# Kernel optimization log

Measured on AMD Instinct MI355X. Metric: run time of the kernel, lower is better.

## Reference

```python
import jax, jax.numpy as jnp
import numpy as np

B, T, D, H = 32, 1024, 512, 512


def setup_inputs() -> dict:
    key = jax.random.key(0)
    ks = jax.random.split(key, 9)
    K = 1.0 / np.sqrt(H)
    u = lambda k, s: jax.random.uniform(k, s, jnp.float32, -K, K)
    return {
        "x": jax.random.normal(ks[0], (B, T, D), jnp.float32),
        "w_ih_fw": u(ks[1], (3 * H, D)),
        "w_hh_fw": u(ks[2], (3 * H, H)),
        "b_ih_fw": u(ks[3], (3 * H,)),
        "b_hh_fw": u(ks[4], (3 * H,)),
        "w_ih_bw": u(ks[5], (3 * H, D)),
        "w_hh_bw": u(ks[6], (3 * H, H)),
        "b_ih_bw": u(ks[7], (3 * H,)),
        "b_hh_bw": u(ks[8], (3 * H,)),
    }


def _gru_scan(x, w_ih, w_hh, b_ih, b_hh, reverse):
    # x: (B, T, D) -> precompute input projections for all steps: (T, B, 3H)
    b, t, d = x.shape
    h_dim = w_hh.shape[1]
    ih = jnp.einsum("btd,gd->tbg", x, w_ih) + b_ih

    def step(h, ih_t):
        hh = h @ w_hh.T + b_hh  # (B, 3H)
        r = jax.nn.sigmoid(ih_t[:, :h_dim] + hh[:, :h_dim])
        z = jax.nn.sigmoid(ih_t[:, h_dim:2 * h_dim] + hh[:, h_dim:2 * h_dim])
        n = jnp.tanh(ih_t[:, 2 * h_dim:] + r * hh[:, 2 * h_dim:])
        h_new = (1.0 - z) * n + z * h
        return h_new, h_new

    h0 = jnp.zeros((b, h_dim), x.dtype)
    h_last, ys = jax.lax.scan(step, h0, ih, reverse=reverse)
    # ys: (T, B, H), aligned to original time indices even when reverse=True
    return jnp.transpose(ys, (1, 0, 2)), h_last


def reference(x, w_ih_fw, w_hh_fw, b_ih_fw, b_hh_fw, w_ih_bw, w_hh_bw, b_ih_bw, b_hh_bw):
    out_fw, h_fw = _gru_scan(x, w_ih_fw, w_hh_fw, b_ih_fw, b_hh_fw, reverse=False)
    out_bw, h_bw = _gru_scan(x, w_ih_bw, w_hh_bw, b_ih_bw, b_hh_bw, reverse=True)
    outputs = jnp.concatenate([out_fw, out_bw], axis=-1)  # (B, T, 2H)
    return outputs, h_fw, h_bw
```

## Files before the change

### kernel.cpp

```cpp
#include <hip/hip_runtime.h>


#define T_LEN 1024
#define B_SZ  32
#define D_SZ  512
#define H_SZ  512
#define NWG_DIR 32
#define JW 16
#define NTHR 512

typedef __attribute__((ext_vector_type(8))) _Float16 half8;
typedef __attribute__((ext_vector_type(4))) float f32x4;
typedef __attribute__((ext_vector_type(4))) int int4v;

__device__ __forceinline__ _Float16 f2h(float f) { return (_Float16)f; }
__device__ __forceinline__ float sigm_f(float v) {
  return __builtin_amdgcn_rcpf(1.f + __expf(-v));
}
__device__ __forceinline__ float tanh_f(float v) {
  return 1.f - 2.f * __builtin_amdgcn_rcpf(1.f + __expf(2.f * v));
}
__device__ __forceinline__ void bar_lgkm() {
  asm volatile("s_waitcnt lgkmcnt(0)\ns_barrier" ::: "memory");
}

__global__ __launch_bounds__(NTHR, 2)
void gru2_persistent(const float* __restrict__ x,
                     const float* __restrict__ wih_fw, const float* __restrict__ whh_fw,
                     const float* __restrict__ bih_fw, const float* __restrict__ bhh_fw,
                     const float* __restrict__ wih_bw, const float* __restrict__ whh_bw,
                     const float* __restrict__ bih_bw, const float* __restrict__ bhh_bw,
                     float* __restrict__ out,
                     unsigned long long* __restrict__ hex64,
                     unsigned* __restrict__ flags)
{
  __shared__ float Cp[24 * 272];
  __shared__ float biasLds[96];
  __shared__ unsigned long long hLds64[B_SZ * 4];
  unsigned* hLds = (unsigned*)hLds64;

  const int bid  = blockIdx.x;
  const int dir  = bid >> 5;
  const int g    = bid & 31;
  const int tid  = threadIdx.x;
  const int wave = tid >> 6;
  const int lane = tid & 63;

  const float* wih = dir ? wih_bw : wih_fw;
  const float* whh = dir ? whh_bw : whh_fw;
  const float* bih = dir ? bih_bw : bih_fw;
  const float* bhh = dir ? bhh_bw : bhh_fw;

  if (tid < 48) {
    int grow = (tid >> 4) * H_SZ + g * JW + (tid & 15);
    biasLds[tid]      = bih[grow];
    biasLds[48 + tid] = bhh[grow];
  }

  const bool isHh = (wave >= 4);
  const int  wv   = wave & 3;
  const int  wm   = wv & 1;
  const int  kh   = wv >> 1;

  half8 Bf[3][8];
  {
    const float* W = isHh ? whh : wih;
    #pragma unroll
    for (int gam = 0; gam < 3; ++gam) {
      const int row = gam * H_SZ + g * JW + (lane & 15);
      #pragma unroll
      for (int i = 0; i < 8; ++i) {
        const float* src = W + (size_t)row * D_SZ + (kh * 8 + i) * 32 + ((lane >> 4) << 3);
        float4 v0 = *(const float4*)(src);
        float4 v1 = *(const float4*)(src + 4);
        half8 b;
        b[0]=f2h(v0.x); b[1]=f2h(v0.y); b[2]=f2h(v0.z); b[3]=f2h(v0.w);
        b[4]=f2h(v1.x); b[5]=f2h(v1.y); b[6]=f2h(v1.z); b[7]=f2h(v1.w);
        Bf[gam][i] = b;
      }
    }
  }

  const int arow = wm * 16 + (lane & 15);
  const int koff = (lane >> 4) << 3;

  float4 xn[16];
  if (!isHh) {
    const int t0 = dir ? (T_LEN - 1) : 0;
    const float* base = x + ((size_t)arow * T_LEN + t0) * D_SZ + kh * 256 + koff;
    #pragma unroll
    for (int i = 0; i < 8; ++i) {
      xn[2*i]   = *(const float4*)(base + i * 32);
      xn[2*i+1] = *(const float4*)(base + i * 32 + 4);
    }
  }
  __syncthreads();

  float hreg = 0.f;
  const int gb = tid >> 4;
  const int gj = tid & 15;
  float* hlast = out + (size_t)B_SZ * T_LEN * (2 * H_SZ) + (size_t)dir * B_SZ * H_SZ;
  const unsigned* flbase = flags + (size_t)dir * NWG_DIR;

  for (int s = 0; s < T_LEN; ++s) {
    const int t = dir ? (T_LEN - 1 - s) : s;
    const bool hasNext = (s + 1 < T_LEN);

    f32x4 acc[3] = {{0.f,0.f,0.f,0.f},{0.f,0.f,0.f,0.f},{0.f,0.f,0.f,0.f}};

    if (!isHh) {
      half8 a[8];
      #pragma unroll
      for (int i = 0; i < 8; ++i) {
        float4 u = xn[2*i], w = xn[2*i+1];
        half8 h;
        h[0]=f2h(u.x); h[1]=f2h(u.y); h[2]=f2h(u.z); h[3]=f2h(u.w);
        h[4]=f2h(w.x); h[5]=f2h(w.y); h[6]=f2h(w.z); h[7]=f2h(w.w);
        a[i] = h;
      }
      if (hasNext) {
        const int tn = dir ? (T_LEN - 2 - s) : (s + 1);
        const float* base = x + ((size_t)arow * T_LEN + tn) * D_SZ + kh * 256 + koff;
        #pragma unroll
        for (int i = 0; i < 8; ++i) {
          xn[2*i]   = *(const float4*)(base + i * 32);
          xn[2*i+1] = *(const float4*)(base + i * 32 + 4);
        }
      }
      #pragma unroll
      for (int i = 0; i < 8; ++i)
        #pragma unroll
        for (int gam = 0; gam < 3; ++gam)
          acc[gam] = __builtin_amdgcn_mfma_f32_16x16x32_f16(a[i], Bf[gam][i], acc[gam], 0, 0, 0);
    } else if (s > 0) {
      for (;;) {
        unsigned v = (lane < NWG_DIR)
            ? __hip_atomic_load(&flbase[lane], __ATOMIC_RELAXED,
                                __HIP_MEMORY_SCOPE_AGENT)
            : 0xFFFFFFFFu;
        if (__all(v >= (unsigned)s)) break;
      }
      const char* p0 = (const char*)hex64
          + (((size_t)dir * 2 + ((s - 1) & 1)) * (B_SZ * 128)) * 8
          + (size_t)arow * 1024 + (size_t)kh * 512 + (size_t)koff * 2;
      int4v hv[8];
      asm volatile(
        "global_load_dwordx4 %0, %8, off sc0 sc1\n\t"
        "global_load_dwordx4 %1, %8, off offset:64 sc0 sc1\n\t"
        "global_load_dwordx4 %2, %8, off offset:128 sc0 sc1\n\t"
        "global_load_dwordx4 %3, %8, off offset:192 sc0 sc1\n\t"
        "global_load_dwordx4 %4, %8, off offset:256 sc0 sc1\n\t"
        "global_load_dwordx4 %5, %8, off offset:320 sc0 sc1\n\t"
        "global_load_dwordx4 %6, %8, off offset:384 sc0 sc1\n\t"
        "global_load_dwordx4 %7, %8, off offset:448 sc0 sc1\n\t"
        "s_waitcnt vmcnt(0)"
        : "=&v"(hv[0]), "=&v"(hv[1]), "=&v"(hv[2]), "=&v"(hv[3]),
          "=&v"(hv[4]), "=&v"(hv[5]), "=&v"(hv[6]), "=&v"(hv[7])
        : "v"(p0) : "memory");
      __builtin_amdgcn_sched_barrier(0);
      #pragma unroll
      for (int i = 0; i < 8; ++i) {
        half8 a = __builtin_bit_cast(half8, hv[i]);
        #pragma unroll
        for (int gam = 0; gam < 3; ++gam)
          acc[gam] = __builtin_amdgcn_mfma_f32_16x16x32_f16(a, Bf[gam][i], acc[gam], 0, 0, 0);
      }
    }

    {
      const int src = isHh ? 1 : 0;
      #pragma unroll
      for (int gam = 0; gam < 3; ++gam) {
        float* cp = Cp + (size_t)(((src*2 + kh)*3 + gam)*2 + wm) * 272
                       + ((lane >> 4) << 2) * 17 + (lane & 15);
        #pragma unroll
        for (int vv2 = 0; vv2 < 4; ++vv2) cp[vv2 * 17] = acc[gam][vv2];
      }
    }
    bar_lgkm();

    float hnS;
    {
      const int mb = gb >> 4, rb = gb & 15;
      float sih[3], shh[3];
      #pragma unroll
      for (int gam = 0; gam < 3; ++gam) {
        float aih = 0.f, ahh = 0.f;
        #pragma unroll
        for (int q = 0; q < 2; ++q) {
          aih += Cp[(size_t)(((0*2+q)*3+gam)*2 + mb) * 272 + rb * 17 + gj];
          ahh += Cp[(size_t)(((1*2+q)*3+gam)*2 + mb) * 272 + rb * 17 + gj];
        }
        sih[gam] = aih + biasLds[gam * 16 + gj];
        shh[gam] = ahh + biasLds[48 + gam * 16 + gj];
      }
      const float r = sigm_f(sih[0] + shh[0]);
      const float z = sigm_f(sih[1] + shh[1]);
      const float n = tanh_f(sih[2] + r * shh[2]);
      const float hn = (1.f - z) * n + z * hreg;
      hreg = hn;
      hnS = hn;

      const float hother = __shfl_xor(hn, 1);
      if ((gj & 1) == 0) {
        union { unsigned u; _Float16 h[2]; } pr;
        pr.h[0] = f2h(hn); pr.h[1] = f2h(hother);
        hLds[gb * 8 + (gj >> 1)] = pr.u;
      }
      if (!isHh) {
        out[((size_t)gb * T_LEN + t) * (2 * H_SZ) + dir * H_SZ + g * JW + gj] = hn;
        if (s == T_LEN - 1) hlast[gb * H_SZ + g * JW + gj] = hn;
      }
    }
    bar_lgkm();

    if (wave == 4) {
      const size_t pb = ((size_t)dir * 2 + (s & 1)) * (B_SZ * 128);
      #pragma unroll
      for (int i = 0; i < 2; ++i) {
        const int id2 = i * 64 + lane;
        const int gbp = id2 >> 2, jp = id2 & 3;
        __hip_atomic_store(&hex64[pb + (size_t)gbp * 128 + g * 4 + jp],
                           hLds64[gbp * 4 + jp],
                           __ATOMIC_RELAXED, __HIP_MEMORY_SCOPE_AGENT);
      }
      asm volatile("s_waitcnt vmcnt(0)" ::: "memory");
      if (lane == 0)
        __hip_atomic_store((unsigned*)&flags[(size_t)dir * NWG_DIR + g],
                           (unsigned)(s + 1),
                           __ATOMIC_RELAXED, __HIP_MEMORY_SCOPE_AGENT);
    }
    if (isHh) {
      out[((size_t)gb * T_LEN + t) * (2 * H_SZ) + dir * H_SZ + g * JW + gj] = hnS;
      if (s == T_LEN - 1) hlast[gb * H_SZ + g * JW + gj] = hnS;
    }
  }
}

extern "C" void kernel_launch(void* const* d_in, const int* in_sizes, int n_in,
                              void* d_out, int out_size, void* d_ws, size_t ws_size,
                              hipStream_t stream) {
  const float* x      = (const float*)d_in[0];
  const float* wih_fw = (const float*)d_in[1];
  const float* whh_fw = (const float*)d_in[2];
  const float* bih_fw = (const float*)d_in[3];
  const float* bhh_fw = (const float*)d_in[4];
  const float* wih_bw = (const float*)d_in[5];
  const float* whh_bw = (const float*)d_in[6];
  const float* bih_bw = (const float*)d_in[7];
  const float* bhh_bw = (const float*)d_in[8];
  float* out = (float*)d_out;

  const size_t FLAGS_BYTES = 256;
  const size_t HEX_BYTES   = (size_t)2 * 2 * B_SZ * 128 * sizeof(unsigned long long);
  if (ws_size < FLAGS_BYTES + HEX_BYTES) return;

  unsigned* flags = (unsigned*)d_ws;
  unsigned long long* hex64 = (unsigned long long*)((char*)d_ws + FLAGS_BYTES);

  hipMemsetAsync(flags, 0, FLAGS_BYTES, stream);
  gru2_persistent<<<dim3(64), dim3(NTHR), 0, stream>>>(
      x, wih_fw, whh_fw, bih_fw, bhh_fw, wih_bw, whh_bw, bih_bw, bhh_bw,
      out, hex64, flags);
}
```

Baseline: 4.861 ms.

## Publish hidden state directly from registers and poll flags with one wave

Each step's fp16 hidden-state chunk is now packed with lane shuffles and written straight to global memory as 16-byte stores in a new fragment-friendly layout. This removes the LDS staging buffer and the single-wave copy-out stage. Only wave 4 polls the cross-workgroup flags, with a short sleep between polls, and it releases the other hh waves through a shared-memory token, so fewer waves hit the flag cache lines. The flag store is moved after a combined vmcnt/lgkmcnt barrier. This trades a lighter handoff for an extra intra-block spin and a vmcnt wait before every barrier.

```diff
diff --git a/kernel.cpp b/kernel.cpp
--- a/kernel.cpp
+++ b/kernel.cpp
@@ -31,13 +31,12 @@
                      const float* __restrict__ wih_bw, const float* __restrict__ whh_bw,
                      const float* __restrict__ bih_bw, const float* __restrict__ bhh_bw,
                      float* __restrict__ out,
-                     unsigned long long* __restrict__ hex64,
+                     char* __restrict__ hexF,
                      unsigned* __restrict__ flags)
 {
   __shared__ float Cp[24 * 272];
   __shared__ float biasLds[96];
-  __shared__ unsigned long long hLds64[B_SZ * 4];
-  unsigned* hLds = (unsigned*)hLds64;
+  __shared__ int tok;
 
   const int bid  = blockIdx.x;
   const int dir  = bid >> 5;
@@ -51,6 +50,7 @@
   const float* bih = dir ? bih_bw : bih_fw;
   const float* bhh = dir ? bhh_bw : bhh_fw;
 
+  if (tid == 0) tok = 0;
   if (tid < 48) {
     int grow = (tid >> 4) * H_SZ + g * JW + (tid & 15);
     biasLds[tid]      = bih[grow];
@@ -101,6 +101,7 @@
   const int gj = tid & 15;
   float* hlast = out + (size_t)B_SZ * T_LEN * (2 * H_SZ) + (size_t)dir * B_SZ * H_SZ;
   const unsigned* flbase = flags + (size_t)dir * NWG_DIR;
+  char* const exbase = hexF + (size_t)dir * 2 * 32768;
 
   for (int s = 0; s < T_LEN; ++s) {
     const int t = dir ? (T_LEN - 1 - s) : s;
@@ -133,30 +134,27 @@
         for (int gam = 0; gam < 3; ++gam)
           acc[gam] = __builtin_amdgcn_mfma_f32_16x16x32_f16(a[i], Bf[gam][i], acc[gam], 0, 0, 0);
     } else if (s > 0) {
-      for (;;) {
-        unsigned v = (lane < NWG_DIR)
-            ? __hip_atomic_load(&flbase[lane], __ATOMIC_RELAXED,
-                                __HIP_MEMORY_SCOPE_AGENT)
-            : 0xFFFFFFFFu;
-        if (__all(v >= (unsigned)s)) break;
-      }
-      const char* p0 = (const char*)hex64
-          + (((size_t)dir * 2 + ((s - 1) & 1)) * (B_SZ * 128)) * 8
-          + (size_t)arow * 1024 + (size_t)kh * 512 + (size_t)koff * 2;
+      if (wave == 4) {
+        for (;;) {
+          unsigned v = (lane < NWG_DIR)
+              ? __hip_atomic_load(&flbase[lane], __ATOMIC_RELAXED,
+                                  __HIP_MEMORY_SCOPE_AGENT)
+              : 0xFFFFFFFFu;
+          if (__all(v >= (unsigned)s)) break;
+          __builtin_amdgcn_s_sleep(1);
+        }
+        if (lane == 0) *((volatile int*)&tok) = s;
+      } else {
+        while (*((volatile int*)&tok) < s) __builtin_amdgcn_s_sleep(1);
+      }
+      const char* pb = exbase + (size_t)((s - 1) & 1) * 32768;
+      const char* a0 = pb + ((size_t)(kh * 32 + (lane >> 4)) * 512) + (size_t)arow * 16;
       int4v hv[8];
-      asm volatile(
-        "global_load_dwordx4 %0, %8, off sc0 sc1\n\t"
-        "global_load_dwordx4 %1, %8, off offset:64 sc0 sc1\n\t"
-        "global_load_dwordx4 %2, %8, off offset:128 sc0 sc1\n\t"
-        "global_load_dwordx4 %3, %8, off offset:192 sc0 sc1\n\t"
-        "global_load_dwordx4 %4, %8, off offset:256 sc0 sc1\n\t"
-        "global_load_dwordx4 %5, %8, off offset:320 sc0 sc1\n\t"
-        "global_load_dwordx4 %6, %8, off offset:384 sc0 sc1\n\t"
-        "global_load_dwordx4 %7, %8, off offset:448 sc0 sc1\n\t"
-        "s_waitcnt vmcnt(0)"
-        : "=&v"(hv[0]), "=&v"(hv[1]), "=&v"(hv[2]), "=&v"(hv[3]),
-          "=&v"(hv[4]), "=&v"(hv[5]), "=&v"(hv[6]), "=&v"(hv[7])
-        : "v"(p0) : "memory");
+      #pragma unroll
+      for (int i = 0; i < 8; ++i)
+        asm volatile("global_load_dwordx4 %0, %1, off sc0 sc1"
+                     : "=&v"(hv[i]) : "v"(a0 + (size_t)i * 2048));
+      asm volatile("s_waitcnt vmcnt(0)" ::: "memory");
       __builtin_amdgcn_sched_barrier(0);
       #pragma unroll
       for (int i = 0; i < 8; ++i) {
@@ -201,39 +199,27 @@
       hreg = hn;
       hnS = hn;
 
-      const float hother = __shfl_xor(hn, 1);
-      if ((gj & 1) == 0) {
-        union { unsigned u; _Float16 h[2]; } pr;
-        pr.h[0] = f2h(hn); pr.h[1] = f2h(hother);
-        hLds[gb * 8 + (gj >> 1)] = pr.u;
-      }
-      if (!isHh) {
-        out[((size_t)gb * T_LEN + t) * (2 * H_SZ) + dir * H_SZ + g * JW + gj] = hn;
-        if (s == T_LEN - 1) hlast[gb * H_SZ + g * JW + gj] = hn;
-      }
-    }
-    bar_lgkm();
-
-    if (wave == 4) {
-      const size_t pb = ((size_t)dir * 2 + (s & 1)) * (B_SZ * 128);
-      #pragma unroll
-      for (int i = 0; i < 2; ++i) {
-        const int id2 = i * 64 + lane;
-        const int gbp = id2 >> 2, jp = id2 & 3;
-        __hip_atomic_store(&hex64[pb + (size_t)gbp * 128 + g * 4 + jp],
-                           hLds64[gbp * 4 + jp],
-                           __ATOMIC_RELAXED, __HIP_MEMORY_SCOPE_AGENT);
-      }
-      asm volatile("s_waitcnt vmcnt(0)" ::: "memory");
-      if (lane == 0)
-        __hip_atomic_store((unsigned*)&flags[(size_t)dir * NWG_DIR + g],
-                           (unsigned)(s + 1),
-                           __ATOMIC_RELAXED, __HIP_MEMORY_SCOPE_AGENT);
-    }
-    if (isHh) {
-      out[((size_t)gb * T_LEN + t) * (2 * H_SZ) + dir * H_SZ + g * JW + gj] = hnS;
-      if (s == T_LEN - 1) hlast[gb * H_SZ + g * JW + gj] = hnS;
-    }
+      const unsigned hu = (unsigned)__builtin_bit_cast(unsigned short, f2h(hn));
+      unsigned v0 = hu | ((unsigned)__shfl_xor((int)hu, 1) << 16);
+      unsigned v1 = (unsigned)__shfl_xor((int)v0, 2);
+      unsigned v2 = (unsigned)__shfl_xor((int)v0, 4);
+      unsigned v3 = (unsigned)__shfl_xor((int)v1, 4);
+      if ((lane & 7) == 0) {
+        int4v pk; pk[0] = (int)v0; pk[1] = (int)v1; pk[2] = (int)v2; pk[3] = (int)v3;
+        char* dst = exbase + (size_t)(s & 1) * 32768
+                  + (size_t)(2 * g + ((lane >> 3) & 1)) * 512
+                  + (size_t)gb * 16;
+        asm volatile("global_store_dwordx4 %0, %1, off sc0 sc1"
+                     :: "v"(dst), "v"(pk) : "memory");
+      }
+    }
+    asm volatile("s_waitcnt vmcnt(0) lgkmcnt(0)\ns_barrier" ::: "memory");
+    if (tid == 0)
+      __hip_atomic_store((unsigned*)&flags[(size_t)dir * NWG_DIR + g],
+                         (unsigned)(s + 1),
+                         __ATOMIC_RELAXED, __HIP_MEMORY_SCOPE_AGENT);
+    out[((size_t)gb * T_LEN + t) * (2 * H_SZ) + dir * H_SZ + g * JW + gj] = hnS;
+    if (s == T_LEN - 1) hlast[gb * H_SZ + g * JW + gj] = hnS;
   }
 }
 
@@ -252,14 +238,14 @@
   float* out = (float*)d_out;
 
   const size_t FLAGS_BYTES = 256;
-  const size_t HEX_BYTES   = (size_t)2 * 2 * B_SZ * 128 * sizeof(unsigned long long);
+  const size_t HEX_BYTES   = (size_t)2 * 2 * 64 * 32 * 16;
   if (ws_size < FLAGS_BYTES + HEX_BYTES) return;
 
   unsigned* flags = (unsigned*)d_ws;
-  unsigned long long* hex64 = (unsigned long long*)((char*)d_ws + FLAGS_BYTES);
+  char* hexF = (char*)d_ws + FLAGS_BYTES;
 
   hipMemsetAsync(flags, 0, FLAGS_BYTES, stream);
   gru2_persistent<<<dim3(64), dim3(NTHR), 0, stream>>>(
       x, wih_fw, whh_fw, bih_fw, bhh_fw, wih_bw, whh_bw, bih_bw, bhh_bw,
-      out, hex64, flags);
-}
+      out, hexF, flags);
+}
```

Measured after the change: 4.778 ms. About the same (-1.7%).

## Publish hidden state directly from gate threads and defer x prefetch past flag

Applied to the files above, without the earlier changes.

Gate-computing threads now write their packed fp16 hidden-state pairs straight to the global exchange buffer with atomic stores. This removes the LDS staging and the single-wave copy-out before the step flag is raised. All threads wait on their own stores, then one thread publishes the flag after the barrier. The output writes and the next-step x prefetch move after the flag publication, shortening the critical path between steps. The cost is more scattered small global stores, and a per-thread vmcnt wait that also stalls on earlier output stores.

```diff
diff --git a/kernel.cpp b/kernel.cpp
--- a/kernel.cpp
+++ b/kernel.cpp
@@ -31,13 +31,11 @@
                      const float* __restrict__ wih_bw, const float* __restrict__ whh_bw,
                      const float* __restrict__ bih_bw, const float* __restrict__ bhh_bw,
                      float* __restrict__ out,
-                     unsigned long long* __restrict__ hex64,
+                     unsigned* __restrict__ hexu,
                      unsigned* __restrict__ flags)
 {
   __shared__ float Cp[24 * 272];
   __shared__ float biasLds[96];
-  __shared__ unsigned long long hLds64[B_SZ * 4];
-  unsigned* hLds = (unsigned*)hLds64;
 
   const int bid  = blockIdx.x;
   const int dir  = bid >> 5;
@@ -83,11 +81,12 @@
 
   const int arow = wm * 16 + (lane & 15);
   const int koff = (lane >> 4) << 3;
+  const float* const xwavebase = x + (size_t)arow * T_LEN * D_SZ + kh * 256 + koff;
 
   float4 xn[16];
   if (!isHh) {
     const int t0 = dir ? (T_LEN - 1) : 0;
-    const float* base = x + ((size_t)arow * T_LEN + t0) * D_SZ + kh * 256 + koff;
+    const float* base = xwavebase + (size_t)t0 * D_SZ;
     #pragma unroll
     for (int i = 0; i < 8; ++i) {
       xn[2*i]   = *(const float4*)(base + i * 32);
@@ -117,15 +116,6 @@
         h[0]=f2h(u.x); h[1]=f2h(u.y); h[2]=f2h(u.z); h[3]=f2h(u.w);
         h[4]=f2h(w.x); h[5]=f2h(w.y); h[6]=f2h(w.z); h[7]=f2h(w.w);
         a[i] = h;
-      }
-      if (hasNext) {
-        const int tn = dir ? (T_LEN - 2 - s) : (s + 1);
-        const float* base = x + ((size_t)arow * T_LEN + tn) * D_SZ + kh * 256 + koff;
-        #pragma unroll
-        for (int i = 0; i < 8; ++i) {
-          xn[2*i]   = *(const float4*)(base + i * 32);
-          xn[2*i+1] = *(const float4*)(base + i * 32 + 4);
-        }
       }
       #pragma unroll
       for (int i = 0; i < 8; ++i)
@@ -140,9 +130,9 @@
             : 0xFFFFFFFFu;
         if (__all(v >= (unsigned)s)) break;
       }
-      const char* p0 = (const char*)hex64
-          + (((size_t)dir * 2 + ((s - 1) & 1)) * (B_SZ * 128)) * 8
-          + (size_t)arow * 1024 + (size_t)kh * 512 + (size_t)koff * 2;
+      const char* p0 = (const char*)hexu
+          + (((size_t)dir * 2 + ((s - 1) & 1)) * (B_SZ * (H_SZ / 2))) * 4
+          + (size_t)arow * (H_SZ * 2) + (size_t)(kh * 256 + koff) * 2;
       int4v hv[8];
       asm volatile(
         "global_load_dwordx4 %0, %8, off sc0 sc1\n\t"
@@ -205,34 +195,28 @@
       if ((gj & 1) == 0) {
         union { unsigned u; _Float16 h[2]; } pr;
         pr.h[0] = f2h(hn); pr.h[1] = f2h(hother);
-        hLds[gb * 8 + (gj >> 1)] = pr.u;
-      }
-      if (!isHh) {
-        out[((size_t)gb * T_LEN + t) * (2 * H_SZ) + dir * H_SZ + g * JW + gj] = hn;
-        if (s == T_LEN - 1) hlast[gb * H_SZ + g * JW + gj] = hn;
-      }
-    }
+        unsigned* hp = hexu + ((size_t)dir * 2 + (s & 1)) * (B_SZ * (H_SZ / 2))
+                     + (size_t)gb * (H_SZ / 2) + (g * JW + gj) / 2;
+        __hip_atomic_store(hp, pr.u, __ATOMIC_RELAXED, __HIP_MEMORY_SCOPE_AGENT);
+      }
+    }
+    asm volatile("s_waitcnt vmcnt(0)" ::: "memory");
     bar_lgkm();
-
-    if (wave == 4) {
-      const size_t pb = ((size_t)dir * 2 + (s & 1)) * (B_SZ * 128);
-      #pragma unroll
-      for (int i = 0; i < 2; ++i) {
-        const int id2 = i * 64 + lane;
-        const int gbp = id2 >> 2, jp = id2 & 3;
-        __hip_atomic_store(&hex64[pb + (size_t)gbp * 128 + g * 4 + jp],
-                           hLds64[gbp * 4 + jp],
-                           __ATOMIC_RELAXED, __HIP_MEMORY_SCOPE_AGENT);
-      }
-      asm volatile("s_waitcnt vmcnt(0)" ::: "memory");
-      if (lane == 0)
-        __hip_atomic_store((unsigned*)&flags[(size_t)dir * NWG_DIR + g],
-                           (unsigned)(s + 1),
-                           __ATOMIC_RELAXED, __HIP_MEMORY_SCOPE_AGENT);
-    }
-    if (isHh) {
-      out[((size_t)gb * T_LEN + t) * (2 * H_SZ) + dir * H_SZ + g * JW + gj] = hnS;
-      if (s == T_LEN - 1) hlast[gb * H_SZ + g * JW + gj] = hnS;
+    if (tid == 0)
+      __hip_atomic_store((unsigned*)&flags[(size_t)dir * NWG_DIR + g],
+                         (unsigned)(s + 1),
+                         __ATOMIC_RELAXED, __HIP_MEMORY_SCOPE_AGENT);
+
+    out[((size_t)gb * T_LEN + t) * (2 * H_SZ) + dir * H_SZ + g * JW + gj] = hnS;
+    if (s == T_LEN - 1) hlast[gb * H_SZ + g * JW + gj] = hnS;
+    if (!isHh && hasNext) {
+      const int tn = dir ? (T_LEN - 2 - s) : (s + 1);
+      const float* base = xwavebase + (size_t)tn * D_SZ;
+      #pragma unroll
+      for (int i = 0; i < 8; ++i) {
+        xn[2*i]   = *(const float4*)(base + i * 32);
+        xn[2*i+1] = *(const float4*)(base + i * 32 + 4);
+      }
     }
   }
 }
@@ -252,14 +236,14 @@
   float* out = (float*)d_out;
 
   const size_t FLAGS_BYTES = 256;
-  const size_t HEX_BYTES   = (size_t)2 * 2 * B_SZ * 128 * sizeof(unsigned long long);
+  const size_t HEX_BYTES   = (size_t)2 * 2 * B_SZ * (H_SZ / 2) * sizeof(unsigned);
   if (ws_size < FLAGS_BYTES + HEX_BYTES) return;
 
   unsigned* flags = (unsigned*)d_ws;
-  unsigned long long* hex64 = (unsigned long long*)((char*)d_ws + FLAGS_BYTES);
+  unsigned* hexu  = (unsigned*)((char*)d_ws + FLAGS_BYTES);
 
   hipMemsetAsync(flags, 0, FLAGS_BYTES, stream);
   gru2_persistent<<<dim3(64), dim3(NTHR), 0, stream>>>(
       x, wih_fw, whh_fw, bih_fw, bhh_fw, wih_bw, whh_bw, bih_bw, bhh_bw,
-      out, hex64, flags);
-}
+      out, hexu, flags);
+}
```

Result: faster. 4.423 ms (-9.0%).
